# Kernel tuning notes

Hardware: AMD Instinct MI355X
Metric: run time of the kernel (lower is better)

## Reference

```python
import jax, jax.numpy as jnp
import numpy as np

MARGIN = 0.3
EPS = 1e-6  # torch.nn.functional.pairwise_distance eps


def setup_inputs() -> dict:
    key = jax.random.key(0)
    k1, k2 = jax.random.split(key)
    B, D, C = 8192, 256, 512
    embeddings = jax.random.normal(k1, (B, D), dtype=jnp.float32)
    labels = jax.random.randint(k2, (B,), 0, C, dtype=jnp.int64)
    return {"embeddings": embeddings, "labels": labels}


def reference(embeddings, labels):
    B = embeddings.shape[0]
    # pairwise squared L2 via GEMM
    dot = embeddings @ embeddings.T                      # [B, B]
    sq = jnp.diag(dot)[:, None] + jnp.diag(dot)[None, :] - 2.0 * dot
    dist_sq = jnp.clip(sq, 0.0)

    same = labels[:, None] == labels[None, :]            # [B, B] bool
    eye = jnp.eye(B, dtype=bool)
    pos_mask = same & ~eye
    neg_mask = ~same

    valid = pos_mask.any(axis=1) & neg_mask.any(axis=1)  # [B]
    INF = dist_sq.max() + 1.0

    hardest_pos_idx = jnp.argmax(dist_sq * pos_mask.astype(dist_sq.dtype), axis=1)
    hardest_neg_idx = jnp.argmin(dist_sq + same.astype(dist_sq.dtype) * INF, axis=1)

    a = embeddings
    p = embeddings[hardest_pos_idx]
    n = embeddings[hardest_neg_idx]
    # torch pairwise_distance: ||x1 - x2 + eps||_2
    d_ap = jnp.linalg.norm(a - p + EPS, axis=1)
    d_an = jnp.linalg.norm(a - n + EPS, axis=1)
    per_anchor = jnp.maximum(d_ap - d_an + MARGIN, 0.0)

    v = valid.astype(per_anchor.dtype)
    n_valid = v.sum()
    loss = jnp.where(n_valid > 0, (per_anchor * v).sum() / jnp.maximum(n_valid, 1.0), 0.0)
    return loss
```

## Files before the change

### kernel.cpp

```cpp
#include <hip/hip_runtime.h>
#include <math.h>

#define NB 8192
#define ND 256
#define NSJ 8
#define JSLICE (NB / NSJ)
#define MARGIN_F 0.3f
#define EPS_F 1e-6f
#define BIAS_F 512.0f
#define NFIN 2048

typedef __attribute__((ext_vector_type(8))) short bf16x8;
typedef __attribute__((ext_vector_type(4))) float f32x4;

__device__ __forceinline__ unsigned short f2bf(float x) {
    unsigned int u = __float_as_uint(x);
    return (unsigned short)((u + 0x7fffu + ((u >> 16) & 1u)) >> 16);
}

__device__ __forceinline__ void gld16(const void* g, void* l) {
    __builtin_amdgcn_global_load_lds(
        (const __attribute__((address_space(1))) void*)g,
        (__attribute__((address_space(3))) void*)l, 16, 0, 0);
}

__global__ __launch_bounds__(512) void prep_k(const float* __restrict__ emb,
                                              unsigned short* __restrict__ ehi,
                                              float* __restrict__ sqnb,
                                              unsigned int* __restrict__ pos_key,
                                              unsigned int* __restrict__ neg_key) {
    __shared__ float sm[8][16];
    const int tid = threadIdx.x;
    const int tk = tid >> 6;
    const int lane = tid & 63;
    const int q = lane >> 4;
    const int lx = lane & 15;
    const int row = blockIdx.x * 16 + lx;
    const int k = tk * 32 + q * 8;

    const float4 v0 = *reinterpret_cast<const float4*>(&emb[(size_t)row * ND + k]);
    const float4 v1 = *reinterpret_cast<const float4*>(&emb[(size_t)row * ND + k + 4]);
    ushort4 h0, h1;
    h0.x = f2bf(v0.x); h0.y = f2bf(v0.y); h0.z = f2bf(v0.z); h0.w = f2bf(v0.w);
    h1.x = f2bf(v1.x); h1.y = f2bf(v1.y); h1.z = f2bf(v1.z); h1.w = f2bf(v1.w);
    *reinterpret_cast<ushort4*>(&ehi[(size_t)blockIdx.x * 4096 + tid * 8])     = h0;
    *reinterpret_cast<ushort4*>(&ehi[(size_t)blockIdx.x * 4096 + tid * 8 + 4]) = h1;

    if (tid >= 32 && tid < 48) pos_key[blockIdx.x * 16 + (tid - 32)] = 0u;
    if (tid >= 48 && tid < 64) neg_key[blockIdx.x * 16 + (tid - 48)] = 0xFFFFFFFFu;

    float s = v0.x * v0.x + v0.y * v0.y + v0.z * v0.z + v0.w * v0.w
            + v1.x * v1.x + v1.y * v1.y + v1.z * v1.z + v1.w * v1.w;
    s += __shfl_xor(s, 16, 64);
    s += __shfl_xor(s, 32, 64);
    if (q == 0) sm[tk][lx] = s;
    __syncthreads();
    if (tid < 16) {
        float t = 0.0f;
#pragma unroll
        for (int wv = 0; wv < 8; ++wv) t += sm[wv][tid];
        sqnb[blockIdx.x * 16 + tid] = t + BIAS_F;
    }
}

template <bool DIAG>
__device__ __forceinline__ void mine_tile(
        const f32x4 (&acc)[4][4], const float* __restrict__ sqj_s,
        const int* __restrict__ lbl_j_s, const int* __restrict__ lbl_i_s,
        int jb, unsigned (&pmax)[16], unsigned (&nmin)[16],
        int wr, int wc, int q, int lx) {
    int lblc[4]; float sqjc[4]; unsigned enc[4];
#pragma unroll
    for (int tc = 0; tc < 4; ++tc) {
        const int colb = wc + tc * 16 + lx;
        lblc[tc] = lbl_j_s[colb];
        sqjc[tc] = sqj_s[colb];
        enc[tc] = 8191u - (unsigned)(jb + colb);
    }
#pragma unroll
    for (int tr = 0; tr < 4; ++tr) {
#pragma unroll
        for (int reg = 0; reg < 4; ++reg) {
            const int r = tr * 4 + reg;
            const int rowb = wr + tr * 16 + q * 4 + reg;
            const int lab = lbl_i_s[rowb];
#pragma unroll
            for (int tc = 0; tc < 4; ++tc) {
                const float v = fmaf(-2.0f, acc[tr][tc][reg], sqjc[tc]);
                const unsigned key = (__float_as_uint(v) & 0xFFFFE000u) | enc[tc];
                const bool same = (lblc[tc] == lab);
                bool pc = same;
                if (DIAG) pc = same && ((wc + tc * 16 + lx) != rowb);
                const unsigned pk = pc ? key : 0u;
                const unsigned nk = same ? 0xFFFFFFFFu : key;
                pmax[r] = pmax[r] >= pk ? pmax[r] : pk;
                nmin[r] = nmin[r] <= nk ? nmin[r] : nk;
            }
        }
    }
}

__global__ __launch_bounds__(256, 2) void pair_k(
        const unsigned short* __restrict__ ehi, const float* __restrict__ sqnb,
        const int* __restrict__ labels,
        unsigned int* __restrict__ pos_key, unsigned int* __restrict__ neg_key) {
    __shared__ short Bsh[64 * 512];
    __shared__ int   lbl_i_s[128];
    __shared__ int   lbl_j_s[128];
    __shared__ float sqj_s[128];

    const int tid = threadIdx.x;
    const int w = tid >> 6;
    const int lane = tid & 63;
    const int q = lane >> 4;
    const int lx = lane & 15;
    const int i_base = blockIdx.x * 128;
    const int slice = blockIdx.y;
    const int wr = (w & 1) * 64;
    const int wc = (w >> 1) * 64;
    const int ib16 = i_base >> 4;

    if (tid < 128) lbl_i_s[tid] = labels[i_base + tid];

    bf16x8 areg[4][8];
#pragma unroll
    for (int t = 0; t < 4; ++t)
#pragma unroll
        for (int kb = 0; kb < 8; ++kb)
            areg[t][kb] = *(const bf16x8*)&ehi[
                ((size_t)(ib16 + (w & 1) * 4 + t) * 8 + kb) * 512 + lane * 8];

    unsigned pmax[16], nmin[16];
#pragma unroll
    for (int r = 0; r < 16; ++r) { pmax[r] = 0u; nmin[r] = 0xFFFFFFFFu; }

#pragma unroll 1
    for (int jt = 0; jt < JSLICE / 128; ++jt) {
        const int jb = slice * JSLICE + jt * 128;
        __syncthreads();
        {
            const unsigned short* srcB = ehi + (size_t)(jb >> 4) * 4096;
#pragma unroll
            for (int p = 0; p < 16; ++p)
                gld16(srcB + ((size_t)p * 256 + tid) * 8, Bsh + (p * 256 + tid) * 8);
        }
        if (tid < 128)        sqj_s[tid] = sqnb[jb + tid];
        else                  lbl_j_s[tid - 128] = labels[jb + tid - 128];
        __syncthreads();

        f32x4 acc[4][4];
#pragma unroll
        for (int a = 0; a < 4; ++a)
#pragma unroll
            for (int b = 0; b < 4; ++b) acc[a][b] = (f32x4){0.f, 0.f, 0.f, 0.f};

#pragma unroll
        for (int kb = 0; kb < 8; ++kb) {
            bf16x8 bh[4];
#pragma unroll
            for (int tc = 0; tc < 4; ++tc) {
                const int cs = (w >> 1) * 4 + tc;
                bh[tc] = *(const bf16x8*)&Bsh[(cs * 8 + kb) * 512 + lane * 8];
            }
#pragma unroll
            for (int tr = 0; tr < 4; ++tr)
#pragma unroll
                for (int tc = 0; tc < 4; ++tc)
                    acc[tr][tc] = __builtin_amdgcn_mfma_f32_16x16x32_bf16(
                        areg[tr][kb], bh[tc], acc[tr][tc], 0, 0, 0);
        }

        if (jb == i_base)
            mine_tile<true>(acc, sqj_s, lbl_j_s, lbl_i_s, jb, pmax, nmin, wr, wc, q, lx);
        else
            mine_tile<false>(acc, sqj_s, lbl_j_s, lbl_i_s, jb, pmax, nmin, wr, wc, q, lx);
    }

#pragma unroll
    for (int r = 0; r < 16; ++r) {
        unsigned pm = pmax[r], nm = nmin[r];
#pragma unroll
        for (int mm = 1; mm < 16; mm <<= 1) {
            const unsigned pm2 = __shfl_xor(pm, mm, 64);
            const unsigned nm2 = __shfl_xor(nm, mm, 64);
            pm = pm >= pm2 ? pm : pm2;
            nm = nm <= nm2 ? nm : nm2;
        }
        if (lx == r) {
            const int row = i_base + wr + (r >> 2) * 16 + q * 4 + (r & 3);
            atomicMax(&pos_key[row], pm);
            atomicMin(&neg_key[row], nm);
        }
    }
}

__global__ __launch_bounds__(256) void final_k(
        const float* __restrict__ emb,
        const unsigned int* __restrict__ pos_key, const unsigned int* __restrict__ neg_key,
        float* __restrict__ pbsum, float* __restrict__ pbcnt) {
    __shared__ float ssum[4], scnt[4];
    const int w = threadIdx.x >> 6;
    const int lane = threadIdx.x & 63;
    const int i = blockIdx.x * 4 + w;

    const unsigned pk = pos_key[i], nk = neg_key[i];
    const int pi = 8191 - (int)(pk & 8191u);
    const int ni = 8191 - (int)(nk & 8191u);
    const bool valid = (pk != 0u) && (nk != 0xFFFFFFFFu);

    const float4 av  = *reinterpret_cast<const float4*>(&emb[(size_t)i  * ND + lane * 4]);
    const float4 pvv = *reinterpret_cast<const float4*>(&emb[(size_t)pi * ND + lane * 4]);
    const float4 nvv = *reinterpret_cast<const float4*>(&emb[(size_t)ni * ND + lane * 4]);
    float sap, san;
    {
        const float d0 = av.x - pvv.x + EPS_F, d1 = av.y - pvv.y + EPS_F;
        const float d2 = av.z - pvv.z + EPS_F, d3 = av.w - pvv.w + EPS_F;
        sap = d0 * d0 + d1 * d1 + d2 * d2 + d3 * d3;
        const float e0 = av.x - nvv.x + EPS_F, e1 = av.y - nvv.y + EPS_F;
        const float e2 = av.z - nvv.z + EPS_F, e3 = av.w - nvv.w + EPS_F;
        san = e0 * e0 + e1 * e1 + e2 * e2 + e3 * e3;
    }
#pragma unroll
    for (int m = 32; m; m >>= 1) {
        sap += __shfl_down(sap, m, 64);
        san += __shfl_down(san, m, 64);
    }
    if (lane == 0) {
        const float per = fmaxf(sqrtf(sap) - sqrtf(san) + MARGIN_F, 0.0f);
        ssum[w] = valid ? per : 0.0f;
        scnt[w] = valid ? 1.0f : 0.0f;
    }
    __syncthreads();
    if (threadIdx.x == 0) {
        pbsum[blockIdx.x] = ssum[0] + ssum[1] + ssum[2] + ssum[3];
        pbcnt[blockIdx.x] = scnt[0] + scnt[1] + scnt[2] + scnt[3];
    }
}

__global__ __launch_bounds__(256) void reduce_k(const float* __restrict__ pbsum,
                                                const float* __restrict__ pbcnt,
                                                float* __restrict__ out) {
    __shared__ float fs[4], fc[4];
    const int tid = threadIdx.x;
    float s = 0.0f, c = 0.0f;
#pragma unroll
    for (int r = 0; r < NFIN / 256; ++r) {
        s += pbsum[r * 256 + tid];
        c += pbcnt[r * 256 + tid];
    }
#pragma unroll
    for (int m = 32; m; m >>= 1) { s += __shfl_down(s, m, 64); c += __shfl_down(c, m, 64); }
    const int wv = tid >> 6, lane = tid & 63;
    if (lane == 0) { fs[wv] = s; fc[wv] = c; }
    __syncthreads();
    if (tid == 0) {
        const float S = fs[0] + fs[1] + fs[2] + fs[3];
        const float C = fc[0] + fc[1] + fc[2] + fc[3];
        out[0] = (C > 0.0f) ? (S / fmaxf(C, 1.0f)) : 0.0f;
    }
}

extern "C" void kernel_launch(void* const* d_in, const int* in_sizes, int n_in,
                              void* d_out, int out_size, void* d_ws, size_t ws_size,
                              hipStream_t stream) {
    const float* emb = (const float*)d_in[0];
    const int* labels = (const int*)d_in[1];
    float* out = (float*)d_out;

    char* ws = (char*)d_ws;
    unsigned short* ehi = (unsigned short*)ws;
    float* sqnb = (float*)(ws + (size_t)NB * ND * 2);
    unsigned int* pos_key = (unsigned int*)(sqnb + NB);
    unsigned int* neg_key = pos_key + NB;
    float* pbsum = (float*)(neg_key + NB);
    float* pbcnt = pbsum + NFIN;

    hipLaunchKernelGGL(prep_k, dim3(NB / 16), dim3(512), 0, stream,
                       emb, ehi, sqnb, pos_key, neg_key);
    hipLaunchKernelGGL(pair_k, dim3(NB / 128, NSJ), dim3(256), 0, stream,
                       ehi, sqnb, labels, pos_key, neg_key);
    hipLaunchKernelGGL(final_k, dim3(NFIN), dim3(256), 0, stream,
                       emb, pos_key, neg_key, pbsum, pbcnt);
    hipLaunchKernelGGL(reduce_k, dim3(1), dim3(256), 0, stream, pbsum, pbcnt, out);
}
```

Measured before the change: 139.9 us.

## Stage A tile in LDS once and stream B fragments directly from global

The row (A) tile is loaded once into shared memory and read from LDS each k-step, while the column (B) tiles are now read straight from global memory into registers. Column labels and norms are also read directly from global. This removes the per-tile LDS staging and both per-iteration barriers, and frees the large A register array. In exchange, every wave fetches B from global/L2 with no sharing through LDS, and the global loads sit right in front of the MFMAs with no prefetch. The grid is flattened to 1D with the slice index as the fastest-varying dimension, which groups the blocks that share a row block.

```diff
diff --git a/kernel.cpp b/kernel.cpp
--- a/kernel.cpp
+++ b/kernel.cpp
@@ -3,8 +3,6 @@
 
 #define NB 8192
 #define ND 256
-#define NSJ 8
-#define JSLICE (NB / NSJ)
 #define MARGIN_F 0.3f
 #define EPS_F 1e-6f
 #define BIAS_F 512.0f
@@ -65,18 +63,10 @@
 
 template <bool DIAG>
 __device__ __forceinline__ void mine_tile(
-        const f32x4 (&acc)[4][4], const float* __restrict__ sqj_s,
-        const int* __restrict__ lbl_j_s, const int* __restrict__ lbl_i_s,
-        int jb, unsigned (&pmax)[16], unsigned (&nmin)[16],
+        const f32x4 (&acc)[4][4], const float (&sqjc)[4], const int (&lblc)[4],
+        const unsigned (&enc)[4], const int* __restrict__ lbl_i_s,
+        unsigned (&pmax)[16], unsigned (&nmin)[16],
         int wr, int wc, int q, int lx) {
-    int lblc[4]; float sqjc[4]; unsigned enc[4];
-#pragma unroll
-    for (int tc = 0; tc < 4; ++tc) {
-        const int colb = wc + tc * 16 + lx;
-        lblc[tc] = lbl_j_s[colb];
-        sqjc[tc] = sqj_s[colb];
-        enc[tc] = 8191u - (unsigned)(jb + colb);
-    }
 #pragma unroll
     for (int tr = 0; tr < 4; ++tr) {
 #pragma unroll
@@ -104,49 +94,48 @@
         const unsigned short* __restrict__ ehi, const float* __restrict__ sqnb,
         const int* __restrict__ labels,
         unsigned int* __restrict__ pos_key, unsigned int* __restrict__ neg_key) {
-    __shared__ short Bsh[64 * 512];
+    __shared__ short Ash[64 * 512];
     __shared__ int   lbl_i_s[128];
-    __shared__ int   lbl_j_s[128];
-    __shared__ float sqj_s[128];
 
     const int tid = threadIdx.x;
     const int w = tid >> 6;
     const int lane = tid & 63;
     const int q = lane >> 4;
     const int lx = lane & 15;
-    const int i_base = blockIdx.x * 128;
-    const int slice = blockIdx.y;
+    const int bid = blockIdx.x;
+    const int slice = bid & 7;
+    const int i_base = (bid >> 3) * 128;
     const int wr = (w & 1) * 64;
     const int wc = (w >> 1) * 64;
-    const int ib16 = i_base >> 4;
+    const int sa = (w & 1) * 4;
 
     if (tid < 128) lbl_i_s[tid] = labels[i_base + tid];
 
-    bf16x8 areg[4][8];
-#pragma unroll
-    for (int t = 0; t < 4; ++t)
-#pragma unroll
-        for (int kb = 0; kb < 8; ++kb)
-            areg[t][kb] = *(const bf16x8*)&ehi[
-                ((size_t)(ib16 + (w & 1) * 4 + t) * 8 + kb) * 512 + lane * 8];
+    {
+        const unsigned short* srcA = ehi + (size_t)(i_base >> 4) * 4096;
+#pragma unroll
+        for (int p = 0; p < 16; ++p)
+            gld16(srcA + ((size_t)p * 256 + tid) * 8, Ash + (p * 256 + tid) * 8);
+    }
+    __syncthreads();
 
     unsigned pmax[16], nmin[16];
 #pragma unroll
     for (int r = 0; r < 16; ++r) { pmax[r] = 0u; nmin[r] = 0xFFFFFFFFu; }
 
 #pragma unroll 1
-    for (int jt = 0; jt < JSLICE / 128; ++jt) {
-        const int jb = slice * JSLICE + jt * 128;
-        __syncthreads();
-        {
-            const unsigned short* srcB = ehi + (size_t)(jb >> 4) * 4096;
-#pragma unroll
-            for (int p = 0; p < 16; ++p)
-                gld16(srcB + ((size_t)p * 256 + tid) * 8, Bsh + (p * 256 + tid) * 8);
-        }
-        if (tid < 128)        sqj_s[tid] = sqnb[jb + tid];
-        else                  lbl_j_s[tid - 128] = labels[jb + tid - 128];
-        __syncthreads();
+    for (int jt = 0; jt < 8; ++jt) {
+        const int jb = slice * 1024 + jt * 128;
+        const size_t bbase = (size_t)(jb >> 4) * 4096;
+
+        int lblc[4]; float sqjc[4]; unsigned enc[4];
+#pragma unroll
+        for (int tc = 0; tc < 4; ++tc) {
+            const int colb = wc + tc * 16 + lx;
+            lblc[tc] = labels[jb + colb];
+            sqjc[tc] = sqnb[jb + colb];
+            enc[tc] = 8191u - (unsigned)(jb + colb);
+        }
 
         f32x4 acc[4][4];
 #pragma unroll
@@ -160,20 +149,24 @@
 #pragma unroll
             for (int tc = 0; tc < 4; ++tc) {
                 const int cs = (w >> 1) * 4 + tc;
-                bh[tc] = *(const bf16x8*)&Bsh[(cs * 8 + kb) * 512 + lane * 8];
+                bh[tc] = *(const bf16x8*)&ehi[bbase + ((size_t)cs * 8 + kb) * 512 + lane * 8];
             }
+            bf16x8 ah[4];
+#pragma unroll
+            for (int tr = 0; tr < 4; ++tr)
+                ah[tr] = *(const bf16x8*)&Ash[((sa + tr) * 8 + kb) * 512 + lane * 8];
 #pragma unroll
             for (int tr = 0; tr < 4; ++tr)
 #pragma unroll
                 for (int tc = 0; tc < 4; ++tc)
                     acc[tr][tc] = __builtin_amdgcn_mfma_f32_16x16x32_bf16(
-                        areg[tr][kb], bh[tc], acc[tr][tc], 0, 0, 0);
+                        ah[tr], bh[tc], acc[tr][tc], 0, 0, 0);
         }
 
         if (jb == i_base)
-            mine_tile<true>(acc, sqj_s, lbl_j_s, lbl_i_s, jb, pmax, nmin, wr, wc, q, lx);
+            mine_tile<true>(acc, sqjc, lblc, enc, lbl_i_s, pmax, nmin, wr, wc, q, lx);
         else
-            mine_tile<false>(acc, sqj_s, lbl_j_s, lbl_i_s, jb, pmax, nmin, wr, wc, q, lx);
+            mine_tile<false>(acc, sqjc, lblc, enc, lbl_i_s, pmax, nmin, wr, wc, q, lx);
     }
 
 #pragma unroll
@@ -277,7 +270,7 @@
 
     hipLaunchKernelGGL(prep_k, dim3(NB / 16), dim3(512), 0, stream,
                        emb, ehi, sqnb, pos_key, neg_key);
-    hipLaunchKernelGGL(pair_k, dim3(NB / 128, NSJ), dim3(256), 0, stream,
+    hipLaunchKernelGGL(pair_k, dim3(512), dim3(256), 0, stream,
                        ehi, sqnb, labels, pos_key, neg_key);
     hipLaunchKernelGGL(final_k, dim3(NFIN), dim3(256), 0, stream,
                        emb, pos_key, neg_key, pbsum, pbcnt);
```

Measured after the change: 214.6 us. 1.53x slower.
